# Kernel optimization log

Hardware: AMD Instinct MI355X
Metric: run time of the kernel (lower is better)

Reference implementation:

```python
import jax, jax.numpy as jnp
import numpy as np

N = 200000   # octree nodes at this depth (in_h == out_h for stride=1)
K = 27       # kdim = 3*3*3
C_IN = 32
C_OUT = 32


def setup_inputs() -> dict:
    key = jax.random.key(0)
    k1, k2, k3 = jax.random.split(key, 3)
    data = jax.random.normal(k1, (N, C_IN), dtype=jnp.float32)
    weights = jax.random.normal(k2, (K, C_IN, C_OUT), dtype=jnp.float32) * 0.05
    raw = jax.random.randint(k3, (N, K), 0, N + N // 10)
    neigh = jnp.where(raw < N, raw, -1).astype(jnp.int64)
    return {"data": data, "weights": weights, "neigh": neigh}


def reference(data, weights, neigh):
    # gather neighbor features, zero-filled where neigh == -1
    valid = neigh >= 0                                 # [N, K]
    safe_idx = jnp.where(valid, neigh, 0)
    gathered = jnp.where(valid[..., None], data[safe_idx], 0.0)  # [N, K, C_in]
    # buffered GEMM: out[n, o] = sum_{k, c} gathered[n, k, c] * weights[k, c, o]
    out = jnp.einsum('nkc,kco->no', gathered, weights)           # [N, C_out]
    return out
```

## Files before the change

### kernel.cpp

```cpp
#include <hip/hip_runtime.h>
#include <hip/hip_bf16.h>

#define N_NODES 200000
#define KDIM 27
#define C_IN 32
#define C_OUT 32

typedef __bf16 bf16x8 __attribute__((ext_vector_type(8)));
typedef float floatx4 __attribute__((ext_vector_type(4)));
typedef float float4_t __attribute__((ext_vector_type(4)));

__device__ inline bf16x8 zero_bf16x8() {
    bf16x8 z;
#pragma unroll
    for (int i = 0; i < 8; ++i) z[i] = (__bf16)0.0f;
    return z;
}

__global__ __launch_bounds__(256) void convert_data_kernel(
    const float* __restrict__ src, __bf16* __restrict__ dst) {
    int i = blockIdx.x * 256 + threadIdx.x;
    const float4_t* s = (const float4_t*)src;
    float4_t v0 = s[2 * i];
    float4_t v1 = s[2 * i + 1];
    bf16x8 o;
    o[0] = (__bf16)v0[0]; o[1] = (__bf16)v0[1];
    o[2] = (__bf16)v0[2]; o[3] = (__bf16)v0[3];
    o[4] = (__bf16)v1[0]; o[5] = (__bf16)v1[1];
    o[6] = (__bf16)v1[2]; o[7] = (__bf16)v1[3];
    ((bf16x8*)dst)[i] = o;
}

__global__ __launch_bounds__(256) void pack_weights_kernel(
    const float* __restrict__ w, __bf16* __restrict__ wp) {
    int id = blockIdx.x * 256 + threadIdx.x;
    int j = id & 7;
    int l = (id >> 3) & 63;
    int t = (id >> 9) & 1;
    int kk = id >> 10;
    int c = ((l >> 4) << 3) + j;
    int o = t * 16 + (l & 15);
    wp[id] = (__bf16)w[(kk * C_IN + c) * C_OUT + o];
}

__global__ __launch_bounds__(256) void octconv_main_kernel(
    const int* __restrict__ neigh, const __bf16* __restrict__ data_bf,
    const __bf16* __restrict__ wpack, float* __restrict__ out) {
    int tid  = threadIdx.x;
    int wave = tid >> 6;
    int lane = tid & 63;
    int node_base = (blockIdx.x * 4 + wave) * 32;
    int r16  = lane & 15;
    int half = lane >> 4;
    int cb   = half << 3;
    int m0   = node_base + r16;
    int m1   = m0 + 16;

    floatx4 acc00 = {0.f, 0.f, 0.f, 0.f};
    floatx4 acc01 = {0.f, 0.f, 0.f, 0.f};
    floatx4 acc10 = {0.f, 0.f, 0.f, 0.f};
    floatx4 acc11 = {0.f, 0.f, 0.f, 0.f};

    const bf16x8* wp = (const bf16x8*)wpack;

#pragma unroll 3
    for (int kk = 0; kk < KDIM; ++kk) {
        int idx0 = (m0 < N_NODES) ? neigh[m0 * KDIM + kk] : -1;
        int idx1 = (m1 < N_NODES) ? neigh[m1 * KDIM + kk] : -1;

        bf16x8 a0 = zero_bf16x8();
        bf16x8 a1 = zero_bf16x8();
        if (idx0 >= 0) a0 = *(const bf16x8*)(data_bf + ((size_t)idx0 << 5) + cb);
        if (idx1 >= 0) a1 = *(const bf16x8*)(data_bf + ((size_t)idx1 << 5) + cb);

        bf16x8 b0 = wp[(kk * 2 + 0) * 64 + lane];
        bf16x8 b1 = wp[(kk * 2 + 1) * 64 + lane];

        acc00 = __builtin_amdgcn_mfma_f32_16x16x32_bf16(a0, b0, acc00, 0, 0, 0);
        acc01 = __builtin_amdgcn_mfma_f32_16x16x32_bf16(a0, b1, acc01, 0, 0, 0);
        acc10 = __builtin_amdgcn_mfma_f32_16x16x32_bf16(a1, b0, acc10, 0, 0, 0);
        acc11 = __builtin_amdgcn_mfma_f32_16x16x32_bf16(a1, b1, acc11, 0, 0, 0);
    }

#pragma unroll
    for (int r = 0; r < 4; ++r) {
        int row = half * 4 + r;
        int n0 = node_base + row;
        int n1 = n0 + 16;
        if (n0 < N_NODES) {
            out[n0 * C_OUT + r16]      = acc00[r];
            out[n0 * C_OUT + 16 + r16] = acc01[r];
        }
        if (n1 < N_NODES) {
            out[n1 * C_OUT + r16]      = acc10[r];
            out[n1 * C_OUT + 16 + r16] = acc11[r];
        }
    }
}

extern "C" void kernel_launch(void* const* d_in, const int* in_sizes, int n_in,
                              void* d_out, int out_size, void* d_ws, size_t ws_size,
                              hipStream_t stream) {
    const float* data    = (const float*)d_in[0];
    const float* weights = (const float*)d_in[1];
    const int*   neigh   = (const int*)d_in[2];
    float*       out     = (float*)d_out;

    __bf16* data_bf = (__bf16*)d_ws;
    __bf16* wpack   = (__bf16*)((char*)d_ws + (size_t)N_NODES * C_IN * 2);

    hipLaunchKernelGGL(convert_data_kernel, dim3((N_NODES * C_IN / 8 + 255) / 256),
                       dim3(256), 0, stream, data, data_bf);
    hipLaunchKernelGGL(pack_weights_kernel, dim3((KDIM * C_IN * C_OUT + 255) / 256),
                       dim3(256), 0, stream, weights, wpack);
    int blocks = (N_NODES + 127) / 128;
    hipLaunchKernelGGL(octconv_main_kernel, dim3(blocks), dim3(256), 0, stream,
                       neigh, data_bf, wpack, out);
}
```

Measured before the change: 194.7 us.

## Restructure octconv K-reduction to pack four neighbors per MFMA over channel-split data

```diff
diff --git a/kernel.cpp b/kernel.cpp
--- a/kernel.cpp
+++ b/kernel.cpp
@@ -20,81 +20,99 @@
 __global__ __launch_bounds__(256) void convert_data_kernel(
     const float* __restrict__ src, __bf16* __restrict__ dst) {
     int i = blockIdx.x * 256 + threadIdx.x;
-    const float4_t* s = (const float4_t*)src;
-    float4_t v0 = s[2 * i];
-    float4_t v1 = s[2 * i + 1];
-    bf16x8 o;
-    o[0] = (__bf16)v0[0]; o[1] = (__bf16)v0[1];
-    o[2] = (__bf16)v0[2]; o[3] = (__bf16)v0[3];
-    o[4] = (__bf16)v1[0]; o[5] = (__bf16)v1[1];
-    o[6] = (__bf16)v1[2]; o[7] = (__bf16)v1[3];
-    ((bf16x8*)dst)[i] = o;
+    if (i >= N_NODES) return;
+    const float4_t* s = (const float4_t*)(src + (size_t)i * 32);
+    float4_t v[8];
+#pragma unroll
+    for (int j = 0; j < 8; ++j) v[j] = s[j];
+#pragma unroll
+    for (int c = 0; c < 4; ++c) {
+        bf16x8 o;
+        o[0] = (__bf16)v[2*c][0]; o[1] = (__bf16)v[2*c][1];
+        o[2] = (__bf16)v[2*c][2]; o[3] = (__bf16)v[2*c][3];
+        o[4] = (__bf16)v[2*c+1][0]; o[5] = (__bf16)v[2*c+1][1];
+        o[6] = (__bf16)v[2*c+1][2]; o[7] = (__bf16)v[2*c+1][3];
+        ((bf16x8*)dst)[(size_t)c * N_NODES + i] = o;
+    }
 }
 
 __global__ __launch_bounds__(256) void pack_weights_kernel(
     const float* __restrict__ w, __bf16* __restrict__ wp) {
     int id = blockIdx.x * 256 + threadIdx.x;
+    if (id >= 56 * 64 * 8) return;
     int j = id & 7;
-    int l = (id >> 3) & 63;
-    int t = (id >> 9) & 1;
-    int kk = id >> 10;
-    int c = ((l >> 4) << 3) + j;
-    int o = t * 16 + (l & 15);
-    wp[id] = (__bf16)w[(kk * C_IN + c) * C_OUT + o];
+    int lane = (id >> 3) & 63;
+    int g = id >> 9;
+    int tt = g & 1;
+    int rest = g >> 1;
+    int t = rest % 7;
+    int c = rest / 7;
+    int kk = 4 * t + (lane >> 4);
+    int ch = 8 * c + j;
+    int o  = tt * 16 + (lane & 15);
+    wp[id] = (kk < KDIM) ? (__bf16)w[((size_t)kk * C_IN + ch) * C_OUT + o] : (__bf16)0.0f;
 }
 
-__global__ __launch_bounds__(256) void octconv_main_kernel(
-    const int* __restrict__ neigh, const __bf16* __restrict__ data_bf,
+__global__ __launch_bounds__(128) void octconv_main_kernel(
+    const int* __restrict__ neigh, const __bf16* __restrict__ data_q,
     const __bf16* __restrict__ wpack, float* __restrict__ out) {
     int tid  = threadIdx.x;
     int wave = tid >> 6;
     int lane = tid & 63;
-    int node_base = (blockIdx.x * 4 + wave) * 32;
-    int r16  = lane & 15;
-    int half = lane >> 4;
-    int cb   = half << 3;
-    int m0   = node_base + r16;
-    int m1   = m0 + 16;
+    int node_base = (blockIdx.x * 2 + wave) * 32;
+    int r16 = lane & 15;
+    int q   = lane >> 4;
+
+    int n0 = node_base + r16;
+    int n1 = n0 + 16;
+
+    const int* np0 = neigh + (size_t)n0 * KDIM + q;
+    const int* np1 = neigh + (size_t)n1 * KDIM + q;
+    int it0[7], it1[7];
+#pragma unroll
+    for (int t = 0; t < 6; ++t) {
+        it0[t] = __builtin_nontemporal_load(np0 + 4 * t);
+        it1[t] = __builtin_nontemporal_load(np1 + 4 * t);
+    }
+    it0[6] = (q == 3) ? -1 : __builtin_nontemporal_load(np0 + 24);
+    it1[6] = (q == 3) ? -1 : __builtin_nontemporal_load(np1 + 24);
 
     floatx4 acc00 = {0.f, 0.f, 0.f, 0.f};
     floatx4 acc01 = {0.f, 0.f, 0.f, 0.f};
     floatx4 acc10 = {0.f, 0.f, 0.f, 0.f};
     floatx4 acc11 = {0.f, 0.f, 0.f, 0.f};
 
-    const bf16x8* wp = (const bf16x8*)wpack;
+    const bf16x8* wp8 = (const bf16x8*)wpack;
 
-#pragma unroll 3
-    for (int kk = 0; kk < KDIM; ++kk) {
-        int idx0 = (m0 < N_NODES) ? neigh[m0 * KDIM + kk] : -1;
-        int idx1 = (m1 < N_NODES) ? neigh[m1 * KDIM + kk] : -1;
-
-        bf16x8 a0 = zero_bf16x8();
-        bf16x8 a1 = zero_bf16x8();
-        if (idx0 >= 0) a0 = *(const bf16x8*)(data_bf + ((size_t)idx0 << 5) + cb);
-        if (idx1 >= 0) a1 = *(const bf16x8*)(data_bf + ((size_t)idx1 << 5) + cb);
-
-        bf16x8 b0 = wp[(kk * 2 + 0) * 64 + lane];
-        bf16x8 b1 = wp[(kk * 2 + 1) * 64 + lane];
-
-        acc00 = __builtin_amdgcn_mfma_f32_16x16x32_bf16(a0, b0, acc00, 0, 0, 0);
-        acc01 = __builtin_amdgcn_mfma_f32_16x16x32_bf16(a0, b1, acc01, 0, 0, 0);
-        acc10 = __builtin_amdgcn_mfma_f32_16x16x32_bf16(a1, b0, acc10, 0, 0, 0);
-        acc11 = __builtin_amdgcn_mfma_f32_16x16x32_bf16(a1, b1, acc11, 0, 0, 0);
+    for (int c = 0; c < 4; ++c) {
+        const __bf16* region = data_q + (size_t)c * N_NODES * 8;
+#pragma unroll
+        for (int t = 0; t < 7; ++t) {
+            int i0 = it0[t];
+            int i1 = it1[t];
+            bf16x8 a0 = zero_bf16x8();
+            bf16x8 a1 = zero_bf16x8();
+            if (i0 >= 0) a0 = *(const bf16x8*)(region + ((size_t)i0 << 3));
+            if (i1 >= 0) a1 = *(const bf16x8*)(region + ((size_t)i1 << 3));
+            int gb = ((c * 7 + t) * 2) * 64 + lane;
+            bf16x8 b0 = wp8[gb];
+            bf16x8 b1 = wp8[gb + 64];
+            acc00 = __builtin_amdgcn_mfma_f32_16x16x32_bf16(a0, b0, acc00, 0, 0, 0);
+            acc01 = __builtin_amdgcn_mfma_f32_16x16x32_bf16(a0, b1, acc01, 0, 0, 0);
+            acc10 = __builtin_amdgcn_mfma_f32_16x16x32_bf16(a1, b0, acc10, 0, 0, 0);
+            acc11 = __builtin_amdgcn_mfma_f32_16x16x32_bf16(a1, b1, acc11, 0, 0, 0);
+        }
     }
 
 #pragma unroll
     for (int r = 0; r < 4; ++r) {
-        int row = half * 4 + r;
-        int n0 = node_base + row;
-        int n1 = n0 + 16;
-        if (n0 < N_NODES) {
-            out[n0 * C_OUT + r16]      = acc00[r];
-            out[n0 * C_OUT + 16 + r16] = acc01[r];
-        }
-        if (n1 < N_NODES) {
-            out[n1 * C_OUT + r16]      = acc10[r];
-            out[n1 * C_OUT + 16 + r16] = acc11[r];
-        }
+        int row = q * 4 + r;
+        float* p0 = out + (size_t)(node_base + row) * C_OUT + r16;
+        float* p1 = out + (size_t)(node_base + 16 + row) * C_OUT + r16;
+        __builtin_nontemporal_store(acc00[r], p0);
+        __builtin_nontemporal_store(acc01[r], p0 + 16);
+        __builtin_nontemporal_store(acc10[r], p1);
+        __builtin_nontemporal_store(acc11[r], p1 + 16);
     }
 }
 
@@ -106,14 +124,13 @@
     const int*   neigh   = (const int*)d_in[2];
     float*       out     = (float*)d_out;
 
-    __bf16* data_bf = (__bf16*)d_ws;
-    __bf16* wpack   = (__bf16*)((char*)d_ws + (size_t)N_NODES * C_IN * 2);
+    __bf16* data_q = (__bf16*)d_ws;
+    __bf16* wpack  = (__bf16*)((char*)d_ws + (size_t)N_NODES * C_IN * 2);
 
-    hipLaunchKernelGGL(convert_data_kernel, dim3((N_NODES * C_IN / 8 + 255) / 256),
-                       dim3(256), 0, stream, data, data_bf);
-    hipLaunchKernelGGL(pack_weights_kernel, dim3((KDIM * C_IN * C_OUT + 255) / 256),
+    hipLaunchKernelGGL(convert_data_kernel, dim3((N_NODES + 255) / 256),
+                       dim3(256), 0, stream, data, data_q);
+    hipLaunchKernelGGL(pack_weights_kernel, dim3((56 * 64 * 8 + 255) / 256),
                        dim3(256), 0, stream, weights, wpack);
-    int blocks = (N_NODES + 127) / 128;
-    hipLaunchKernelGGL(octconv_main_kernel, dim3(blocks), dim3(256), 0, stream,
-                       neigh, data_bf, wpack, out);
+    hipLaunchKernelGGL(octconv_main_kernel, dim3(N_NODES / 64), dim3(128), 0, stream,
+                       neigh, data_q, wpack, out);
 }
```

Measured after the change: 259.4 us. 1.33x slower.

## Software-pipeline neighbor index and gather loads, merge prep kernels into one launch

Applied to the files above, without the earlier changes.

```diff
diff --git a/kernel.cpp b/kernel.cpp
--- a/kernel.cpp
+++ b/kernel.cpp
@@ -3,8 +3,12 @@
 
 #define N_NODES 200000
 #define KDIM 27
+#define TAPS_PAD 28
+#define NGROUPS 14
 #define C_IN 32
 #define C_OUT 32
+#define CONV_BLOCKS 3125
+#define PACK_BLOCKS 112
 
 typedef __bf16 bf16x8 __attribute__((ext_vector_type(8)));
 typedef float floatx4 __attribute__((ext_vector_type(4)));
@@ -17,70 +21,110 @@
     return z;
 }
 
-__global__ __launch_bounds__(256) void convert_data_kernel(
-    const float* __restrict__ src, __bf16* __restrict__ dst) {
-    int i = blockIdx.x * 256 + threadIdx.x;
-    const float4_t* s = (const float4_t*)src;
-    float4_t v0 = s[2 * i];
-    float4_t v1 = s[2 * i + 1];
-    bf16x8 o;
-    o[0] = (__bf16)v0[0]; o[1] = (__bf16)v0[1];
-    o[2] = (__bf16)v0[2]; o[3] = (__bf16)v0[3];
-    o[4] = (__bf16)v1[0]; o[5] = (__bf16)v1[1];
-    o[6] = (__bf16)v1[2]; o[7] = (__bf16)v1[3];
-    ((bf16x8*)dst)[i] = o;
-}
-
-__global__ __launch_bounds__(256) void pack_weights_kernel(
+__global__ __launch_bounds__(256) void aux_kernel(
+    const float* __restrict__ src, __bf16* __restrict__ dst,
     const float* __restrict__ w, __bf16* __restrict__ wp) {
-    int id = blockIdx.x * 256 + threadIdx.x;
-    int j = id & 7;
-    int l = (id >> 3) & 63;
-    int t = (id >> 9) & 1;
-    int kk = id >> 10;
-    int c = ((l >> 4) << 3) + j;
-    int o = t * 16 + (l & 15);
-    wp[id] = (__bf16)w[(kk * C_IN + c) * C_OUT + o];
+    if (blockIdx.x < CONV_BLOCKS) {
+        int i = blockIdx.x * 256 + threadIdx.x;
+        const float4_t* s = (const float4_t*)src;
+        float4_t v0 = s[2 * i];
+        float4_t v1 = s[2 * i + 1];
+        bf16x8 o;
+        o[0] = (__bf16)v0[0]; o[1] = (__bf16)v0[1];
+        o[2] = (__bf16)v0[2]; o[3] = (__bf16)v0[3];
+        o[4] = (__bf16)v1[0]; o[5] = (__bf16)v1[1];
+        o[6] = (__bf16)v1[2]; o[7] = (__bf16)v1[3];
+        ((bf16x8*)dst)[i] = o;
+    } else {
+        int id = (blockIdx.x - CONV_BLOCKS) * 256 + threadIdx.x;
+        if (id >= TAPS_PAD * 2 * 64 * 8) return;
+        int j = id & 7;
+        int lane = (id >> 3) & 63;
+        int g = id >> 9;
+        int tt = g & 1;
+        int kk = g >> 1;
+        int c = ((lane >> 4) << 3) + j;
+        int o = tt * 16 + (lane & 15);
+        wp[id] = (kk < KDIM) ? (__bf16)w[((size_t)kk * C_IN + c) * C_OUT + o] : (__bf16)0.0f;
+    }
 }
 
 __global__ __launch_bounds__(256) void octconv_main_kernel(
     const int* __restrict__ neigh, const __bf16* __restrict__ data_bf,
     const __bf16* __restrict__ wpack, float* __restrict__ out) {
     int tid  = threadIdx.x;
-    int wave = tid >> 6;
     int lane = tid & 63;
-    int node_base = (blockIdx.x * 4 + wave) * 32;
+    int wave_id = blockIdx.x * 4 + (tid >> 6);
+    int node_base = wave_id * 32;
     int r16  = lane & 15;
     int half = lane >> 4;
     int cb   = half << 3;
-    int m0   = node_base + r16;
-    int m1   = m0 + 16;
+    int m0 = node_base + r16;
+    int m1 = m0 + 16;
+    bool v0 = m0 < N_NODES;
+    bool v1 = m1 < N_NODES;
+    const int* np0 = neigh + (size_t)m0 * KDIM;
+    const int* np1 = neigh + (size_t)m1 * KDIM;
+
+    int   i0[2][2], i1[2][2];
+    bf16x8 A0[2][2], A1[2][2];
 
     floatx4 acc00 = {0.f, 0.f, 0.f, 0.f};
     floatx4 acc01 = {0.f, 0.f, 0.f, 0.f};
     floatx4 acc10 = {0.f, 0.f, 0.f, 0.f};
     floatx4 acc11 = {0.f, 0.f, 0.f, 0.f};
 
-    const bf16x8* wp = (const bf16x8*)wpack;
+    const bf16x8* wp8 = (const bf16x8*)wpack;
 
-#pragma unroll 3
-    for (int kk = 0; kk < KDIM; ++kk) {
-        int idx0 = (m0 < N_NODES) ? neigh[m0 * KDIM + kk] : -1;
-        int idx1 = (m1 < N_NODES) ? neigh[m1 * KDIM + kk] : -1;
+#define LOAD_IDX(g)                                                              \
+    {                                                                            \
+        int p_ = (g) & 1;                                                        \
+        _Pragma("unroll")                                                        \
+        for (int u_ = 0; u_ < 2; ++u_) {                                         \
+            int kk_ = 2 * (g) + u_;                                              \
+            bool tv_ = kk_ < KDIM;                                               \
+            i0[p_][u_] = (v0 && tv_) ? __builtin_nontemporal_load(np0 + kk_) : -1; \
+            i1[p_][u_] = (v1 && tv_) ? __builtin_nontemporal_load(np1 + kk_) : -1; \
+        }                                                                        \
+    }
+#define GATHER(g)                                                                \
+    {                                                                            \
+        int p_ = (g) & 1;                                                        \
+        _Pragma("unroll")                                                        \
+        for (int u_ = 0; u_ < 2; ++u_) {                                         \
+            int a_ = i0[p_][u_];                                                 \
+            int b_ = i1[p_][u_];                                                 \
+            bf16x8 x_ = zero_bf16x8();                                           \
+            bf16x8 y_ = zero_bf16x8();                                           \
+            if (a_ >= 0) x_ = *(const bf16x8*)(data_bf + ((size_t)(unsigned)a_ << 5) + cb); \
+            if (b_ >= 0) y_ = *(const bf16x8*)(data_bf + ((size_t)(unsigned)b_ << 5) + cb); \
+            A0[p_][u_] = x_;                                                     \
+            A1[p_][u_] = y_;                                                     \
+        }                                                                        \
+    }
 
-        bf16x8 a0 = zero_bf16x8();
-        bf16x8 a1 = zero_bf16x8();
-        if (idx0 >= 0) a0 = *(const bf16x8*)(data_bf + ((size_t)idx0 << 5) + cb);
-        if (idx1 >= 0) a1 = *(const bf16x8*)(data_bf + ((size_t)idx1 << 5) + cb);
+    LOAD_IDX(0);
+    LOAD_IDX(1);
+    GATHER(0);
 
-        bf16x8 b0 = wp[(kk * 2 + 0) * 64 + lane];
-        bf16x8 b1 = wp[(kk * 2 + 1) * 64 + lane];
-
-        acc00 = __builtin_amdgcn_mfma_f32_16x16x32_bf16(a0, b0, acc00, 0, 0, 0);
-        acc01 = __builtin_amdgcn_mfma_f32_16x16x32_bf16(a0, b1, acc01, 0, 0, 0);
-        acc10 = __builtin_amdgcn_mfma_f32_16x16x32_bf16(a1, b0, acc10, 0, 0, 0);
-        acc11 = __builtin_amdgcn_mfma_f32_16x16x32_bf16(a1, b1, acc11, 0, 0, 0);
+#pragma unroll
+    for (int g = 0; g < NGROUPS; ++g) {
+        if (g + 2 < NGROUPS) LOAD_IDX(g + 2);
+        if (g + 1 < NGROUPS) GATHER(g + 1);
+        int p = g & 1;
+#pragma unroll
+        for (int u = 0; u < 2; ++u) {
+            int kk = 2 * g + u;
+            bf16x8 b0 = wp8[(kk * 2 + 0) * 64 + lane];
+            bf16x8 b1 = wp8[(kk * 2 + 1) * 64 + lane];
+            acc00 = __builtin_amdgcn_mfma_f32_16x16x32_bf16(A0[p][u], b0, acc00, 0, 0, 0);
+            acc01 = __builtin_amdgcn_mfma_f32_16x16x32_bf16(A0[p][u], b1, acc01, 0, 0, 0);
+            acc10 = __builtin_amdgcn_mfma_f32_16x16x32_bf16(A1[p][u], b0, acc10, 0, 0, 0);
+            acc11 = __builtin_amdgcn_mfma_f32_16x16x32_bf16(A1[p][u], b1, acc11, 0, 0, 0);
+        }
     }
+#undef LOAD_IDX
+#undef GATHER
 
 #pragma unroll
     for (int r = 0; r < 4; ++r) {
@@ -88,12 +132,14 @@
         int n0 = node_base + row;
         int n1 = n0 + 16;
         if (n0 < N_NODES) {
-            out[n0 * C_OUT + r16]      = acc00[r];
-            out[n0 * C_OUT + 16 + r16] = acc01[r];
+            float* p0 = out + (size_t)n0 * C_OUT + r16;
+            __builtin_nontemporal_store(acc00[r], p0);
+            __builtin_nontemporal_store(acc01[r], p0 + 16);
         }
         if (n1 < N_NODES) {
-            out[n1 * C_OUT + r16]      = acc10[r];
-            out[n1 * C_OUT + 16 + r16] = acc11[r];
+            float* p1 = out + (size_t)n1 * C_OUT + r16;
+            __builtin_nontemporal_store(acc10[r], p1);
+            __builtin_nontemporal_store(acc11[r], p1 + 16);
         }
     }
 }
@@ -109,11 +155,9 @@
     __bf16* data_bf = (__bf16*)d_ws;
     __bf16* wpack   = (__bf16*)((char*)d_ws + (size_t)N_NODES * C_IN * 2);
 
-    hipLaunchKernelGGL(convert_data_kernel, dim3((N_NODES * C_IN / 8 + 255) / 256),
-                       dim3(256), 0, stream, data, data_bf);
-    hipLaunchKernelGGL(pack_weights_kernel, dim3((KDIM * C_IN * C_OUT + 255) / 256),
-                       dim3(256), 0, stream, weights, wpack);
-    int blocks = (N_NODES + 127) / 128;
-    hipLaunchKernelGGL(octconv_main_kernel, dim3(blocks), dim3(256), 0, stream,
+    hipLaunchKernelGGL(aux_kernel, dim3(CONV_BLOCKS + PACK_BLOCKS), dim3(256), 0, stream,
+                       data, data_bf, weights, wpack);
+
+    hipLaunchKernelGGL(octconv_main_kernel, dim3(1563), dim3(256), 0, stream,
                        neigh, data_bf, wpack, out);
 }
```

New measurement: 207.8 us. 6.7% more time.
